# Kernel tuning notes

Measured on AMD Instinct MI355X. Metric: run time of the kernel, lower is better.

Reference implementation:

```python
import jax, jax.numpy as jnp
import numpy as np

INPUT_SIZE = 128
OUTPUT_SIZE = 128
P_NUM = 16
BATCH = 131072


def setup_inputs() -> dict:
    key = jax.random.key(0)
    k_x, k_c = jax.random.split(key)
    x = jax.random.normal(k_x, (BATCH, INPUT_SIZE), dtype=jnp.float32)
    coef = jax.random.normal(k_c, (OUTPUT_SIZE, INPUT_SIZE, P_NUM), dtype=jnp.float32) * 0.1
    tanh_range = jnp.array(1.0, dtype=jnp.float32)
    return {"x": x, "coef": coef, "tanh_range": tanh_range}


def reference(x, coef, tanh_range):
    # Original: values = tanh(x*t); out[b,o] = sum_i sum_p coef[o,i,p] * values[b,i]
    # Equivalent fused form: (sum_p coef) applied as a single GEMM.
    values = jnp.tanh(x * tanh_range)          # [B, I]
    w = jnp.sum(coef, axis=2)                  # [O, I]
    return jnp.einsum('bi,oi->bo', values, w)  # [B, O]
```

## Files before the change

kernel.cpp:

```cpp
#include <hip/hip_runtime.h>

#define BATCH 131072
#define IN 128
#define OUT 128
#define PNUM 16
#define LDS_PITCH 136

typedef _Float16 f16x8 __attribute__((ext_vector_type(8)));
typedef float f32x4 __attribute__((ext_vector_type(4)));

__device__ __forceinline__ float tanh_fast(float v) {
    float e = __expf(2.0f * v);
    return 1.0f - 2.0f * __builtin_amdgcn_rcpf(e + 1.0f);
}

__global__ __launch_bounds__(256) void prep_w_kernel(const float* __restrict__ coef,
                                                     _Float16* __restrict__ w) {
    int t = blockIdx.x * blockDim.x + threadIdx.x;
    const float4* p = (const float4*)(coef + (size_t)t * PNUM);
    float4 a = p[0], b = p[1], c = p[2], d = p[3];
    float s = (a.x + a.y + a.z + a.w) + (b.x + b.y + b.z + b.w)
            + (c.x + c.y + c.z + c.w) + (d.x + d.y + d.z + d.w);
    w[t] = (_Float16)s;
}

__global__ __launch_bounds__(512, 5) void gemm_tanh_kernel(const float* __restrict__ x,
                                                           const _Float16* __restrict__ w,
                                                           const float* __restrict__ trange,
                                                           float* __restrict__ out) {
    __shared__ _Float16 wlds[OUT * LDS_PITCH];

    const float t = trange[0];
    const int tid  = threadIdx.x;
    const int lane = tid & 63;
    const int wv   = tid >> 6;
    const int m = lane & 15;
    const int q = lane >> 4;

    const size_t row_base = (size_t)blockIdx.x * 128 + (size_t)wv * 16;
    const float* xrow = x + (row_base + m) * IN;

    float4 xv[8];
#pragma unroll
    for (int ks = 0; ks < 4; ++ks) {
        xv[2 * ks]     = *(const float4*)(xrow + ks * 32 + q * 8);
        xv[2 * ks + 1] = *(const float4*)(xrow + ks * 32 + q * 8 + 4);
    }

#pragma unroll
    for (int i = 0; i < 4; ++i) {
        int idx = (i * 512 + tid) * 8;
        int r = idx >> 7;
        int c = idx & 127;
        *(f16x8*)&wlds[r * LDS_PITCH + c] = *(const f16x8*)(w + idx);
    }
    __syncthreads();

    f16x8 af[4];
#pragma unroll
    for (int ks = 0; ks < 4; ++ks) {
        float4 a = xv[2 * ks], b = xv[2 * ks + 1];
        af[ks][0] = (_Float16)tanh_fast(a.x * t);
        af[ks][1] = (_Float16)tanh_fast(a.y * t);
        af[ks][2] = (_Float16)tanh_fast(a.z * t);
        af[ks][3] = (_Float16)tanh_fast(a.w * t);
        af[ks][4] = (_Float16)tanh_fast(b.x * t);
        af[ks][5] = (_Float16)tanh_fast(b.y * t);
        af[ks][6] = (_Float16)tanh_fast(b.z * t);
        af[ks][7] = (_Float16)tanh_fast(b.w * t);
    }

    f32x4 acc[8];
#pragma unroll
    for (int nt = 0; nt < 8; ++nt) acc[nt] = (f32x4){0.f, 0.f, 0.f, 0.f};

#pragma unroll
    for (int ks = 0; ks < 4; ++ks) {
        const int kb = ks * 32 + q * 8;
#pragma unroll
        for (int nt = 0; nt < 8; ++nt) {
            f16x8 bf = *(const f16x8*)&wlds[(nt * 16 + m) * LDS_PITCH + kb];
            acc[nt] = __builtin_amdgcn_mfma_f32_16x16x32_f16(af[ks], bf, acc[nt], 0, 0, 0);
        }
    }

    float* orow = out + (row_base + q * 4) * OUT + m;
#pragma unroll
    for (int nt = 0; nt < 8; ++nt) {
#pragma unroll
        for (int r = 0; r < 4; ++r) {
            orow[(size_t)r * OUT + nt * 16] = acc[nt][r];
        }
    }
}

extern "C" void kernel_launch(void* const* d_in, const int* in_sizes, int n_in,
                              void* d_out, int out_size, void* d_ws, size_t ws_size,
                              hipStream_t stream) {
    const float* x    = (const float*)d_in[0];
    const float* coef = (const float*)d_in[1];
    const float* tr   = (const float*)d_in[2];
    float* out = (float*)d_out;
    _Float16* w = (_Float16*)d_ws;

    prep_w_kernel<<<(OUT * IN) / 256, 256, 0, stream>>>(coef, w);
    gemm_tanh_kernel<<<BATCH / 128, 512, 0, stream>>>(x, w, tr, out);
}
```

Before: 119.5 us.

## Use persistent grid with register-resident weights and prefetched x rows

Replaces the one-tile-per-block kernel with a fixed 512-block persistent grid. Each block processes 8 row tiles in a loop and prefetches the next tile's x while computing the current one. Each wave keeps half of the fp16 weight matrix in registers loaded directly from global memory, which removes the LDS staging and the block barrier. This cuts per-block setup and overlaps loads with MFMA work, at the cost of higher register pressure and fewer resident waves (256 threads, occupancy hint 2). Each wave now also recomputes tanh for its rows, because the two column-half waves share the same rows.

```diff
diff --git a/kernel.cpp b/kernel.cpp
--- a/kernel.cpp
+++ b/kernel.cpp
@@ -4,7 +4,8 @@
 #define IN 128
 #define OUT 128
 #define PNUM 16
-#define LDS_PITCH 136
+#define GRID 512
+#define ITERS 8
 
 typedef _Float16 f16x8 __attribute__((ext_vector_type(8)));
 typedef float f32x4 __attribute__((ext_vector_type(4)));
@@ -24,73 +25,77 @@
     w[t] = (_Float16)s;
 }
 
-__global__ __launch_bounds__(512, 5) void gemm_tanh_kernel(const float* __restrict__ x,
+__global__ __launch_bounds__(256, 2) void gemm_tanh_kernel(const float* __restrict__ x,
                                                            const _Float16* __restrict__ w,
                                                            const float* __restrict__ trange,
                                                            float* __restrict__ out) {
-    __shared__ _Float16 wlds[OUT * LDS_PITCH];
+    const float t = trange[0];
+    const int lane = threadIdx.x & 63;
+    const int wv   = threadIdx.x >> 6;
+    const int m  = lane & 15;
+    const int q  = lane >> 4;
+    const int rg = wv >> 1;
+    const int ch = wv & 1;
 
-    const float t = trange[0];
-    const int tid  = threadIdx.x;
-    const int lane = tid & 63;
-    const int wv   = tid >> 6;
-    const int m = lane & 15;
-    const int q = lane >> 4;
+    f16x8 bf[4][4];
+#pragma unroll
+    for (int nt = 0; nt < 4; ++nt)
+#pragma unroll
+        for (int ks = 0; ks < 4; ++ks)
+            bf[nt][ks] = *(const f16x8*)(w + (size_t)(ch * 64 + nt * 16 + m) * IN + ks * 32 + q * 8);
 
-    const size_t row_base = (size_t)blockIdx.x * 128 + (size_t)wv * 16;
-    const float* xrow = x + (row_base + m) * IN;
+    const size_t row0 = (size_t)blockIdx.x * 32 + rg * 16;
 
     float4 xv[8];
+    {
+        const float* xr = x + (row0 + m) * IN;
 #pragma unroll
-    for (int ks = 0; ks < 4; ++ks) {
-        xv[2 * ks]     = *(const float4*)(xrow + ks * 32 + q * 8);
-        xv[2 * ks + 1] = *(const float4*)(xrow + ks * 32 + q * 8 + 4);
+        for (int ks = 0; ks < 4; ++ks) {
+            xv[2 * ks]     = *(const float4*)(xr + ks * 32 + q * 8);
+            xv[2 * ks + 1] = *(const float4*)(xr + ks * 32 + q * 8 + 4);
+        }
     }
 
 #pragma unroll
-    for (int i = 0; i < 4; ++i) {
-        int idx = (i * 512 + tid) * 8;
-        int r = idx >> 7;
-        int c = idx & 127;
-        *(f16x8*)&wlds[r * LDS_PITCH + c] = *(const f16x8*)(w + idx);
-    }
-    __syncthreads();
+    for (int i = 0; i < ITERS; ++i) {
+        f16x8 af[4];
+#pragma unroll
+        for (int ks = 0; ks < 4; ++ks) {
+            float4 a = xv[2 * ks], b = xv[2 * ks + 1];
+            af[ks][0] = (_Float16)tanh_fast(a.x * t);
+            af[ks][1] = (_Float16)tanh_fast(a.y * t);
+            af[ks][2] = (_Float16)tanh_fast(a.z * t);
+            af[ks][3] = (_Float16)tanh_fast(a.w * t);
+            af[ks][4] = (_Float16)tanh_fast(b.x * t);
+            af[ks][5] = (_Float16)tanh_fast(b.y * t);
+            af[ks][6] = (_Float16)tanh_fast(b.z * t);
+            af[ks][7] = (_Float16)tanh_fast(b.w * t);
+        }
 
-    f16x8 af[4];
+        if (i + 1 < ITERS) {
+            const float* xn = x + (row0 + (size_t)(i + 1) * (GRID * 32) + m) * IN;
 #pragma unroll
-    for (int ks = 0; ks < 4; ++ks) {
-        float4 a = xv[2 * ks], b = xv[2 * ks + 1];
-        af[ks][0] = (_Float16)tanh_fast(a.x * t);
-        af[ks][1] = (_Float16)tanh_fast(a.y * t);
-        af[ks][2] = (_Float16)tanh_fast(a.z * t);
-        af[ks][3] = (_Float16)tanh_fast(a.w * t);
-        af[ks][4] = (_Float16)tanh_fast(b.x * t);
-        af[ks][5] = (_Float16)tanh_fast(b.y * t);
-        af[ks][6] = (_Float16)tanh_fast(b.z * t);
-        af[ks][7] = (_Float16)tanh_fast(b.w * t);
-    }
+            for (int ks = 0; ks < 4; ++ks) {
+                xv[2 * ks]     = *(const float4*)(xn + ks * 32 + q * 8);
+                xv[2 * ks + 1] = *(const float4*)(xn + ks * 32 + q * 8 + 4);
+            }
+        }
 
-    f32x4 acc[8];
+        f32x4 acc[4];
 #pragma unroll
-    for (int nt = 0; nt < 8; ++nt) acc[nt] = (f32x4){0.f, 0.f, 0.f, 0.f};
+        for (int nt = 0; nt < 4; ++nt) acc[nt] = (f32x4){0.f, 0.f, 0.f, 0.f};
+#pragma unroll
+        for (int ks = 0; ks < 4; ++ks)
+#pragma unroll
+            for (int nt = 0; nt < 4; ++nt)
+                acc[nt] = __builtin_amdgcn_mfma_f32_16x16x32_f16(af[ks], bf[nt][ks], acc[nt], 0, 0, 0);
 
+        float* orow = out + (row0 + (size_t)i * (GRID * 32) + q * 4) * OUT + ch * 64 + m;
 #pragma unroll
-    for (int ks = 0; ks < 4; ++ks) {
-        const int kb = ks * 32 + q * 8;
+        for (int nt = 0; nt < 4; ++nt)
 #pragma unroll
-        for (int nt = 0; nt < 8; ++nt) {
-            f16x8 bf = *(const f16x8*)&wlds[(nt * 16 + m) * LDS_PITCH + kb];
-            acc[nt] = __builtin_amdgcn_mfma_f32_16x16x32_f16(af[ks], bf, acc[nt], 0, 0, 0);
-        }
-    }
-
-    float* orow = out + (row_base + q * 4) * OUT + m;
-#pragma unroll
-    for (int nt = 0; nt < 8; ++nt) {
-#pragma unroll
-        for (int r = 0; r < 4; ++r) {
-            orow[(size_t)r * OUT + nt * 16] = acc[nt][r];
-        }
+            for (int r = 0; r < 4; ++r)
+                orow[(size_t)r * OUT + nt * 16] = acc[nt][r];
     }
 }
 
@@ -104,5 +109,5 @@
     _Float16* w = (_Float16*)d_ws;
 
     prep_w_kernel<<<(OUT * IN) / 256, 256, 0, stream>>>(coef, w);
-    gemm_tanh_kernel<<<BATCH / 128, 512, 0, stream>>>(x, w, tr, out);
+    gemm_tanh_kernel<<<GRID, 256, 0, stream>>>(x, w, tr, out);
 }
```

New measurement: 130.5 us. +9.2%, slower.

## Process two 64-row tiles per 256-thread block with next-tile x prefetch

Applied to the files above, without the earlier changes.

The GEMM kernel now runs with 256-thread blocks on a fixed grid of 1024. Each block loops over two 64-row tiles, and the x rows for the next tile are loaded while the current tile's MFMAs run. The aim is to overlap global loads with compute, and the LDS weight pitch is changed from 136 to 132 halves. The trade-off is fewer waves resident per CU. A 132-half pitch also leaves odd rows only 8-byte aligned for the 16-byte LDS vector accesses, which may split them or cause bank conflicts.

```diff
diff --git a/kernel.cpp b/kernel.cpp
--- a/kernel.cpp
+++ b/kernel.cpp
@@ -4,7 +4,9 @@
 #define IN 128
 #define OUT 128
 #define PNUM 16
-#define LDS_PITCH 136
+#define GRID 1024
+#define ITERS 2
+#define LDS_PITCH 132
 
 typedef _Float16 f16x8 __attribute__((ext_vector_type(8)));
 typedef float f32x4 __attribute__((ext_vector_type(4)));
@@ -24,7 +26,7 @@
     w[t] = (_Float16)s;
 }
 
-__global__ __launch_bounds__(512, 5) void gemm_tanh_kernel(const float* __restrict__ x,
+__global__ __launch_bounds__(256, 4) void gemm_tanh_kernel(const float* __restrict__ x,
                                                            const _Float16* __restrict__ w,
                                                            const float* __restrict__ trange,
                                                            float* __restrict__ out) {
@@ -33,64 +35,75 @@
     const float t = trange[0];
     const int tid  = threadIdx.x;
     const int lane = tid & 63;
-    const int wv   = tid >> 6;
+    const int rg   = tid >> 6;
     const int m = lane & 15;
     const int q = lane >> 4;
 
-    const size_t row_base = (size_t)blockIdx.x * 128 + (size_t)wv * 16;
-    const float* xrow = x + (row_base + m) * IN;
+    const size_t blk_row = (size_t)blockIdx.x * (64 * ITERS);
 
     float4 xv[8];
+    {
+        const float* xr = x + (blk_row + rg * 16 + m) * IN;
 #pragma unroll
-    for (int ks = 0; ks < 4; ++ks) {
-        xv[2 * ks]     = *(const float4*)(xrow + ks * 32 + q * 8);
-        xv[2 * ks + 1] = *(const float4*)(xrow + ks * 32 + q * 8 + 4);
+        for (int ks = 0; ks < 4; ++ks) {
+            xv[2 * ks]     = *(const float4*)(xr + ks * 32 + q * 8);
+            xv[2 * ks + 1] = *(const float4*)(xr + ks * 32 + q * 8 + 4);
+        }
     }
 
 #pragma unroll
-    for (int i = 0; i < 4; ++i) {
-        int idx = (i * 512 + tid) * 8;
+    for (int j = 0; j < 8; ++j) {
+        int idx = (j * 256 + tid) * 8;
         int r = idx >> 7;
         int c = idx & 127;
         *(f16x8*)&wlds[r * LDS_PITCH + c] = *(const f16x8*)(w + idx);
     }
     __syncthreads();
 
-    f16x8 af[4];
 #pragma unroll
-    for (int ks = 0; ks < 4; ++ks) {
-        float4 a = xv[2 * ks], b = xv[2 * ks + 1];
-        af[ks][0] = (_Float16)tanh_fast(a.x * t);
-        af[ks][1] = (_Float16)tanh_fast(a.y * t);
-        af[ks][2] = (_Float16)tanh_fast(a.z * t);
-        af[ks][3] = (_Float16)tanh_fast(a.w * t);
-        af[ks][4] = (_Float16)tanh_fast(b.x * t);
-        af[ks][5] = (_Float16)tanh_fast(b.y * t);
-        af[ks][6] = (_Float16)tanh_fast(b.z * t);
-        af[ks][7] = (_Float16)tanh_fast(b.w * t);
-    }
+    for (int i = 0; i < ITERS; ++i) {
+        f16x8 af[4];
+#pragma unroll
+        for (int ks = 0; ks < 4; ++ks) {
+            float4 a = xv[2 * ks], b = xv[2 * ks + 1];
+            af[ks][0] = (_Float16)tanh_fast(a.x * t);
+            af[ks][1] = (_Float16)tanh_fast(a.y * t);
+            af[ks][2] = (_Float16)tanh_fast(a.z * t);
+            af[ks][3] = (_Float16)tanh_fast(a.w * t);
+            af[ks][4] = (_Float16)tanh_fast(b.x * t);
+            af[ks][5] = (_Float16)tanh_fast(b.y * t);
+            af[ks][6] = (_Float16)tanh_fast(b.z * t);
+            af[ks][7] = (_Float16)tanh_fast(b.w * t);
+        }
 
-    f32x4 acc[8];
+        if (i + 1 < ITERS) {
+            const float* xn = x + (blk_row + (i + 1) * 64 + rg * 16 + m) * IN;
 #pragma unroll
-    for (int nt = 0; nt < 8; ++nt) acc[nt] = (f32x4){0.f, 0.f, 0.f, 0.f};
+            for (int ks = 0; ks < 4; ++ks) {
+                xv[2 * ks]     = *(const float4*)(xn + ks * 32 + q * 8);
+                xv[2 * ks + 1] = *(const float4*)(xn + ks * 32 + q * 8 + 4);
+            }
+        }
 
+        f32x4 acc[8];
 #pragma unroll
-    for (int ks = 0; ks < 4; ++ks) {
-        const int kb = ks * 32 + q * 8;
+        for (int nt = 0; nt < 8; ++nt) acc[nt] = (f32x4){0.f, 0.f, 0.f, 0.f};
 #pragma unroll
-        for (int nt = 0; nt < 8; ++nt) {
-            f16x8 bf = *(const f16x8*)&wlds[(nt * 16 + m) * LDS_PITCH + kb];
-            acc[nt] = __builtin_amdgcn_mfma_f32_16x16x32_f16(af[ks], bf, acc[nt], 0, 0, 0);
+        for (int ks = 0; ks < 4; ++ks) {
+            const int kb = ks * 32 + q * 8;
+#pragma unroll
+            for (int nt = 0; nt < 8; ++nt) {
+                f16x8 bf = *(const f16x8*)&wlds[(nt * 16 + m) * LDS_PITCH + kb];
+                acc[nt] = __builtin_amdgcn_mfma_f32_16x16x32_f16(af[ks], bf, acc[nt], 0, 0, 0);
+            }
         }
-    }
 
-    float* orow = out + (row_base + q * 4) * OUT + m;
+        float* orow = out + (blk_row + (size_t)i * 64 + rg * 16 + q * 4) * OUT + m;
 #pragma unroll
-    for (int nt = 0; nt < 8; ++nt) {
+        for (int nt = 0; nt < 8; ++nt)
 #pragma unroll
-        for (int r = 0; r < 4; ++r) {
-            orow[(size_t)r * OUT + nt * 16] = acc[nt][r];
-        }
+            for (int r = 0; r < 4; ++r)
+                orow[(size_t)r * OUT + nt * 16] = acc[nt][r];
     }
 }
 
@@ -104,5 +117,5 @@
     _Float16* w = (_Float16*)d_ws;
 
     prep_w_kernel<<<(OUT * IN) / 256, 256, 0, stream>>>(coef, w);
-    gemm_tanh_kernel<<<BATCH / 128, 512, 0, stream>>>(x, w, tr, out);
+    gemm_tanh_kernel<<<GRID, 256, 0, stream>>>(x, w, tr, out);
 }
```

Result: slower. 124.4 us (+4.1%).
